# Kernel optimization log

Measured on AMD Instinct MI355X. Metric: run time of the kernel, lower is better.

## Reference

```python
import jax, jax.numpy as jnp
import numpy as np

EMBED = 128
HEADS = 32          # embed_dim // 4, forced by fuse Conv2d channel counts
HEAD_DIM = EMBED // HEADS  # 4
WS = (4, 7, 7)
N = WS[0] * WS[1] * WS[2]  # 196 tokens per window
B = 64              # batch * num_windows
SCALE = HEAD_DIM ** -0.5
EPS = 1e-5


def _rel_index():
    d, h, w = WS
    coords = np.stack(np.meshgrid(np.arange(d), np.arange(h), np.arange(w), indexing='ij'))
    flat = coords.reshape(3, -1)                       # [3, N]
    rel = (flat[:, :, None] - flat[:, None, :]).transpose(1, 2, 0).astype(np.int64)  # [N,N,3]
    rel[:, :, 0] += d - 1
    rel[:, :, 1] += h - 1
    rel[:, :, 2] += w - 1
    rel[:, :, 0] *= (2 * h - 1) * (2 * w - 1)
    rel[:, :, 1] *= (2 * w - 1)
    return rel.sum(-1).astype(np.int32)                # [N, N]


def setup_inputs() -> dict:
    key = jax.random.key(0)
    ks = jax.random.split(key, 7)
    d, h, w = WS
    tbl = (2 * d - 1) * (2 * h - 1) * (2 * w - 1)
    return {
        'x_in':      jax.random.normal(ks[0], (B, N, EMBED), dtype=jnp.float32),
        'x_in2':     jax.random.normal(ks[1], (B, N, EMBED), dtype=jnp.float32),
        'qkv_w':     jax.random.normal(ks[2], (3 * EMBED, EMBED), dtype=jnp.float32) * 0.02,
        'proj_w':    jax.random.normal(ks[3], (EMBED, EMBED), dtype=jnp.float32) * 0.02,
        'proj_b':    jnp.zeros((EMBED,), dtype=jnp.float32),
        'rpb_table': jax.random.normal(ks[4], (tbl, HEADS), dtype=jnp.float32) * 0.02,
        'fuse_w':    jax.random.normal(ks[5], (EMBED // 4, EMBED // 2), dtype=jnp.float32) * 0.1,
        'fuse_b':    jnp.zeros((EMBED // 4,), dtype=jnp.float32),
        'rel_idx':   jnp.asarray(_rel_index()),
    }


def _branch(x, qkv_w):
    b, n, c = x.shape
    qkv = (x @ qkv_w.T).reshape(b, n, 3, HEADS, c // HEADS).transpose(2, 0, 3, 1, 4)
    q, k, v = qkv[0] * SCALE, qkv[1], qkv[2]           # [b, H, n, d]
    attn = jnp.einsum('bhnd,bhmd->bhnm', q, k)         # [b, H, n, n]
    return attn, v


def reference(x_in, x_in2, qkv_w, proj_w, proj_b, rpb_table, fuse_w, fuse_b, rel_idx):
    b, n, c = x_in.shape
    attn1, v1 = _branch(x_in, qkv_w)
    attn2, v2 = _branch(x_in2, qkv_w)

    # conv-gated value fusion: Conv2d 1x1 over channel dim (= 2H) + InstanceNorm2d + ReLU + Sigmoid
    vcat = jnp.concatenate([v1, v2], axis=1)           # [b, 2H, n, d]
    v = jnp.einsum('bcnd,oc->bond', vcat, fuse_w) + fuse_b[None, :, None, None]  # [b, H, n, d]
    mu = v.mean(axis=(2, 3), keepdims=True)
    var = v.var(axis=(2, 3), keepdims=True)            # biased, as InstanceNorm2d
    v = (v - mu) * jax.lax.rsqrt(var + EPS)
    v = jax.nn.sigmoid(jax.nn.relu(v))

    # relative position bias: gather [n*n] rows of table -> [H, n, n]
    bias = rpb_table[rel_idx[:n, :n].reshape(-1)].reshape(n, n, HEADS).transpose(2, 0, 1)

    attn = jax.nn.softmax(attn1 + attn2 + bias[None], axis=-1)  # [b, H, n, n]
    x = jnp.einsum('bhnm,bhmd->bhnd', attn, v).transpose(0, 2, 1, 3).reshape(b, n, c)
    return x @ proj_w.T + proj_b
```

## Files before the change

kernel.cpp:

```cpp
#include <hip/hip_runtime.h>
#include <hip/hip_bf16.h>
#include <stdint.h>

#define NB   64
#define NTOK 196
#define NH   32
#define HD   4
#define CE   128
#define NM   38416
#define ROWS 25088

typedef __bf16 bf16x8 __attribute__((ext_vector_type(8)));
typedef float  f32x4  __attribute__((ext_vector_type(4)));

__device__ __forceinline__ float u2f(unsigned short u) {
    union { unsigned int i; float f; } z;
    z.i = ((unsigned int)u) << 16;
    return z.f;
}
__device__ __forceinline__ unsigned short f2u(float f) {
    union { float f; unsigned int i; } z; z.f = f;
    unsigned int x = z.i;
    return (unsigned short)((x + 0x7fffu + ((x >> 16) & 1u)) >> 16);
}

extern "C" __global__ __launch_bounds__(256) void qkv_gemm(
    const float* __restrict__ x1,
    const float* __restrict__ x2,
    const float* __restrict__ qkvw,
    float* __restrict__ Q, float* __restrict__ K, unsigned short* __restrict__ V)
{
    __shared__ alignas(16) unsigned short AT[64][136];
    __shared__ alignas(16) unsigned short BT[64][136];
    const int tid = threadIdx.x;
    const int r0 = blockIdx.x * 64;
    const int j0 = blockIdx.y * 64;

    for (int idx = tid; idx < 2048; idx += 256) {
        int row = idx >> 5, k0 = (idx & 31) << 2;
        int r = r0 + row;
        const float* xp = (r >= 12544) ? x2 : x1;
        int rem = r - ((r >= 12544) ? 12544 : 0);
        float4 v = *(const float4*)&xp[rem * 128 + k0];
        ushort4 u; u.x = f2u(v.x); u.y = f2u(v.y); u.z = f2u(v.z); u.w = f2u(v.w);
        *(ushort4*)&AT[row][k0] = u;
    }
    for (int idx = tid; idx < 2048; idx += 256) {
        int row = idx >> 5, k0 = (idx & 31) << 2;
        float4 v = *(const float4*)&qkvw[(j0 + row) * 128 + k0];
        ushort4 u; u.x = f2u(v.x); u.y = f2u(v.y); u.z = f2u(v.z); u.w = f2u(v.w);
        *(ushort4*)&BT[row][k0] = u;
    }
    __syncthreads();

    const int lane = tid & 63, w = tid >> 6;
    const int wm = (w >> 1) * 32, wn = (w & 1) * 32;
    const int quad = lane >> 4, tcol = lane & 15;

    f32x4 acc[2][2] = {};
#pragma unroll
    for (int ks = 0; ks < 4; ++ks) {
        int k0 = ks * 32 + quad * 8;
        bf16x8 a0 = *(const bf16x8*)&AT[wm + tcol][k0];
        bf16x8 a1 = *(const bf16x8*)&AT[wm + 16 + tcol][k0];
        bf16x8 b0 = *(const bf16x8*)&BT[wn + tcol][k0];
        bf16x8 b1 = *(const bf16x8*)&BT[wn + 16 + tcol][k0];
        acc[0][0] = __builtin_amdgcn_mfma_f32_16x16x32_bf16(a0, b0, acc[0][0], 0, 0, 0);
        acc[0][1] = __builtin_amdgcn_mfma_f32_16x16x32_bf16(a0, b1, acc[0][1], 0, 0, 0);
        acc[1][0] = __builtin_amdgcn_mfma_f32_16x16x32_bf16(a1, b0, acc[1][0], 0, 0, 0);
        acc[1][1] = __builtin_amdgcn_mfma_f32_16x16x32_bf16(a1, b1, acc[1][1], 0, 0, 0);
    }

#pragma unroll
    for (int mi = 0; mi < 2; ++mi) {
#pragma unroll
        for (int ni = 0; ni < 2; ++ni) {
            int jglob = j0 + wn + ni * 16 + tcol;
            int sel = jglob >> 7;
            int jj = jglob & 127;
            int h = jj >> 2, dd = jj & 3;
#pragma unroll
            for (int reg = 0; reg < 4; ++reg) {
                int r = r0 + wm + mi * 16 + quad * 4 + reg;
                int branch = (r >= 12544) ? 1 : 0;
                int rem = r - branch * 12544;
                int b = rem / 196;
                int n = rem - b * 196;
                float v = acc[mi][ni][reg];
                if (sel == 0) {
                    Q[((branch * 64 + b) * 32 + h) * 784 + n * 4 + dd] = v * 0.5f;
                } else if (sel == 1) {
                    K[((branch * 64 + b) * 32 + h) * 784 + n * 4 + dd] = v;
                } else {
                    V[(b * 64 + branch * 32 + h) * 784 + n * 4 + dd] = f2u(v);
                }
            }
        }
    }
}

extern "C" __global__ __launch_bounds__(256) void bias_gather(
    const int* __restrict__ rel_idx, const float* __restrict__ rpb,
    unsigned short* __restrict__ biasT)
{
    const int m = blockIdx.x;
    const int n = threadIdx.x;
    if (n >= 196) return;
    int idx = rel_idx[n * 196 + m];
    const float* row = rpb + idx * 32;
    unsigned short* o = biasT + m * 196 + n;
#pragma unroll
    for (int h = 0; h < 32; ++h)
        o[h * NM] = f2u(row[h]);
}

__device__ __forceinline__ float block_sum(float v, float* red, int tid) {
#pragma unroll
    for (int off = 32; off > 0; off >>= 1) v += __shfl_down(v, off);
    __syncthreads();
    if ((tid & 63) == 0) red[tid >> 6] = v;
    __syncthreads();
    return red[0] + red[1] + red[2] + red[3];
}

__device__ __forceinline__ float act_sig_relu(float x) {
    return x > 0.f ? __fdividef(1.f, 1.f + __expf(-x)) : 0.5f;
}

extern "C" __global__ __launch_bounds__(256) void fuse_kernel(
    const unsigned short* __restrict__ V,
    const float* __restrict__ fuse_w,
    const float* __restrict__ fuse_b,
    float* __restrict__ Vf)
{
    const int b = blockIdx.x, o0 = blockIdx.y * 2;
    const int tid = threadIdx.x;
    __shared__ float fws[2][64];
    __shared__ float red[4];
    if (tid < 128) fws[tid >> 6][tid & 63] = fuse_w[(o0 + (tid >> 6)) * 64 + (tid & 63)];
    __syncthreads();

    const unsigned short* Vb = V + b * 64 * 784;
    float a0[3] = {0.f, 0.f, 0.f}, a1[3] = {0.f, 0.f, 0.f};
    float t0 = 0.f, t1 = 0.f;
    const bool tail = tid < 16;
    for (int c = 0; c < 64; ++c) {
        float w0 = fws[0][c], w1 = fws[1][c];
        const unsigned short* Vc = Vb + c * 784;
#pragma unroll
        for (int k = 0; k < 3; ++k) {
            float x = u2f(Vc[tid + 256 * k]);
            a0[k] = fmaf(w0, x, a0[k]);
            a1[k] = fmaf(w1, x, a1[k]);
        }
        if (tail) {
            float x = u2f(Vc[tid + 768]);
            t0 = fmaf(w0, x, t0);
            t1 = fmaf(w1, x, t1);
        }
    }
    float fb0 = fuse_b[o0], fb1 = fuse_b[o0 + 1];
#pragma unroll
    for (int k = 0; k < 3; ++k) { a0[k] += fb0; a1[k] += fb1; }
    t0 += fb0; t1 += fb1;

    float s0 = a0[0] + a0[1] + a0[2] + (tail ? t0 : 0.f);
    float q0 = a0[0]*a0[0] + a0[1]*a0[1] + a0[2]*a0[2] + (tail ? t0*t0 : 0.f);
    float s1 = a1[0] + a1[1] + a1[2] + (tail ? t1 : 0.f);
    float q1 = a1[0]*a1[0] + a1[1]*a1[1] + a1[2]*a1[2] + (tail ? t1*t1 : 0.f);

    float S0 = block_sum(s0, red, tid);
    float Q0 = block_sum(q0, red, tid);
    float S1 = block_sum(s1, red, tid);
    float Q1 = block_sum(q1, red, tid);

    const float inv = 1.0f / 784.0f;
    float mu0 = S0 * inv, mu1 = S1 * inv;
    float rs0 = rsqrtf(Q0 * inv - mu0 * mu0 + 1e-5f);
    float rs1 = rsqrtf(Q1 * inv - mu1 * mu1 + 1e-5f);

    float* out0 = Vf + (b * 32 + o0) * 784;
    float* out1 = out0 + 784;
#pragma unroll
    for (int k = 0; k < 3; ++k) {
        int e = tid + 256 * k;
        out0[e] = act_sig_relu((a0[k] - mu0) * rs0);
        out1[e] = act_sig_relu((a1[k] - mu1) * rs1);
    }
    if (tail) {
        out0[tid + 768] = act_sig_relu((t0 - mu0) * rs0);
        out1[tid + 768] = act_sig_relu((t1 - mu1) * rs1);
    }
}

extern "C" __global__ __launch_bounds__(256) void attn_kernel(
    const float* __restrict__ Q, const float* __restrict__ K,
    const float* __restrict__ Vf, const unsigned short* __restrict__ biasT,
    unsigned short* __restrict__ Ob)
{
    const int bh = blockIdx.x;
    const int b = bh >> 5, h = bh & 31;
    __shared__ float k1s[196][4];
    __shared__ float k2s[196][4];
    __shared__ float vfs[196][4];
    const int tid = threadIdx.x;
    const int base1 = (b * 32 + h) * 784;
    const int base2 = ((64 + b) * 32 + h) * 784;
    const int basev = (b * 32 + h) * 784;
    for (int idx = tid; idx < 784; idx += 256) {
        (&k1s[0][0])[idx] = K[base1 + idx];
        (&k2s[0][0])[idx] = K[base2 + idx];
        (&vfs[0][0])[idx] = Vf[basev + idx];
    }
    __syncthreads();

    const int n = tid;
    if (n < 196) {
        float4 q1 = *(const float4*)(Q + base1 + n * 4);
        float4 q2 = *(const float4*)(Q + base2 + n * 4);
        const unsigned short* bp = biasT + h * NM + n;
        float S = 0.f, o0 = 0.f, o1 = 0.f, o2 = 0.f, o3 = 0.f;
        for (int m = 0; m < 196; ++m) {
            float4 k1 = *(const float4*)&k1s[m][0];
            float4 k2 = *(const float4*)&k2s[m][0];
            float s = u2f(bp[m * 196]);
            s = fmaf(q1.x, k1.x, fmaf(q1.y, k1.y, fmaf(q1.z, k1.z, fmaf(q1.w, k1.w, s))));
            s = fmaf(q2.x, k2.x, fmaf(q2.y, k2.y, fmaf(q2.z, k2.z, fmaf(q2.w, k2.w, s))));
            float p = __expf(s);
            S += p;
            float4 vv = *(const float4*)&vfs[m][0];
            o0 = fmaf(p, vv.x, o0); o1 = fmaf(p, vv.y, o1);
            o2 = fmaf(p, vv.z, o2); o3 = fmaf(p, vv.w, o3);
        }
        float invS = __fdividef(1.f, S);
        unsigned short* op = Ob + (b * 196 + n) * 128 + h * 4;
        op[0] = f2u(o0 * invS); op[1] = f2u(o1 * invS);
        op[2] = f2u(o2 * invS); op[3] = f2u(o3 * invS);
    }
}

extern "C" __global__ __launch_bounds__(256) void proj_kernel(
    const unsigned short* __restrict__ Ob, const float* __restrict__ projw,
    const float* __restrict__ projb, float* __restrict__ out)
{
    __shared__ alignas(16) unsigned short AT[64][136];
    __shared__ alignas(16) unsigned short BT[64][136];
    const int tid = threadIdx.x;
    const int r0 = blockIdx.x * 64;
    const int j0 = blockIdx.y * 64;

    for (int idx = tid; idx < 1024; idx += 256) {
        int row = idx >> 4, k0 = (idx & 15) << 3;
        *(uint4*)&AT[row][k0] = *(const uint4*)&Ob[(r0 + row) * 128 + k0];
    }
    for (int idx = tid; idx < 2048; idx += 256) {
        int row = idx >> 5, k0 = (idx & 31) << 2;
        float4 v = *(const float4*)&projw[(j0 + row) * 128 + k0];
        ushort4 u; u.x = f2u(v.x); u.y = f2u(v.y); u.z = f2u(v.z); u.w = f2u(v.w);
        *(ushort4*)&BT[row][k0] = u;
    }
    __syncthreads();

    const int lane = tid & 63, w = tid >> 6;
    const int wm = (w >> 1) * 32, wn = (w & 1) * 32;
    const int quad = lane >> 4, tcol = lane & 15;

    f32x4 acc[2][2] = {};
#pragma unroll
    for (int ks = 0; ks < 4; ++ks) {
        int k0 = ks * 32 + quad * 8;
        bf16x8 a0 = *(const bf16x8*)&AT[wm + tcol][k0];
        bf16x8 a1 = *(const bf16x8*)&AT[wm + 16 + tcol][k0];
        bf16x8 b0 = *(const bf16x8*)&BT[wn + tcol][k0];
        bf16x8 b1 = *(const bf16x8*)&BT[wn + 16 + tcol][k0];
        acc[0][0] = __builtin_amdgcn_mfma_f32_16x16x32_bf16(a0, b0, acc[0][0], 0, 0, 0);
        acc[0][1] = __builtin_amdgcn_mfma_f32_16x16x32_bf16(a0, b1, acc[0][1], 0, 0, 0);
        acc[1][0] = __builtin_amdgcn_mfma_f32_16x16x32_bf16(a1, b0, acc[1][0], 0, 0, 0);
        acc[1][1] = __builtin_amdgcn_mfma_f32_16x16x32_bf16(a1, b1, acc[1][1], 0, 0, 0);
    }

#pragma unroll
    for (int mi = 0; mi < 2; ++mi) {
#pragma unroll
        for (int ni = 0; ni < 2; ++ni) {
            int j = j0 + wn + ni * 16 + tcol;
            float pb = projb[j];
#pragma unroll
            for (int reg = 0; reg < 4; ++reg) {
                int r = r0 + wm + mi * 16 + quad * 4 + reg;
                out[r * 128 + j] = acc[mi][ni][reg] + pb;
            }
        }
    }
}

extern "C" void kernel_launch(void* const* d_in, const int* in_sizes, int n_in,
                              void* d_out, int out_size, void* d_ws, size_t ws_size,
                              hipStream_t stream)
{
    const float* x1    = (const float*)d_in[0];
    const float* x2    = (const float*)d_in[1];
    const float* qkvw  = (const float*)d_in[2];
    const float* projw = (const float*)d_in[3];
    const float* projb = (const float*)d_in[4];
    const float* rpb   = (const float*)d_in[5];
    const float* fw    = (const float*)d_in[6];
    const float* fb    = (const float*)d_in[7];
    const int*   rel   = (const int*)d_in[8];
    float* out = (float*)d_out;

    char* w = (char*)d_ws;
    float* Q            = (float*)(w);
    float* K            = (float*)(w + 12845056);
    unsigned short* V   = (unsigned short*)(w + 25690112);
    float* Vf           = (float*)(w + 32112640);
    unsigned short* bT  = (unsigned short*)(w + 38535168);
    unsigned short* Ob  = (unsigned short*)(w + 40993792);

    qkv_gemm   <<<dim3(392, 6), dim3(256), 0, stream>>>(x1, x2, qkvw, Q, K, V);
    bias_gather<<<dim3(196),    dim3(256), 0, stream>>>(rel, rpb, bT);
    fuse_kernel<<<dim3(64, 16), dim3(256), 0, stream>>>(V, fw, fb, Vf);
    attn_kernel<<<dim3(2048),   dim3(256), 0, stream>>>(Q, K, Vf, bT, Ob);
    proj_kernel<<<dim3(196, 2), dim3(256), 0, stream>>>(Ob, projw, projb, out);
}
```

Before: 177.2 us.

## Move attention to bf16 MFMA with packed Q/K and MFMA-layout bias

Rewrites the attention kernel to compute scores and P·V with 16x16x32 bf16 MFMA instructions instead of scalar FMA loops. Q and K from both branches are packed into one 8-wide bf16 row so a single MFMA does the concatenated dot product. The softmax scale and log2e are folded in so exp2 can be used. The bias is prebuilt in MFMA accumulator layout with -inf padding. A ones column in V yields the row sum for normalisation. This trades scalar ALU work and fp32 traffic for matrix-core throughput, at the cost of bf16 precision on Q, K and probabilities, plus an LDS round trip to transpose P.

```diff
diff --git a/kernel.cpp b/kernel.cpp
--- a/kernel.cpp
+++ b/kernel.cpp
@@ -8,10 +8,12 @@
 #define HD   4
 #define CE   128
 #define NM   38416
-#define ROWS 25088
 
 typedef __bf16 bf16x8 __attribute__((ext_vector_type(8)));
 typedef float  f32x4  __attribute__((ext_vector_type(4)));
+
+#define QSCALE 0.7213475204444817f
+#define LOG2E  1.4426950408889634f
 
 __device__ __forceinline__ float u2f(unsigned short u) {
     union { unsigned int i; float f; } z;
@@ -28,7 +30,8 @@
     const float* __restrict__ x1,
     const float* __restrict__ x2,
     const float* __restrict__ qkvw,
-    float* __restrict__ Q, float* __restrict__ K, unsigned short* __restrict__ V)
+    unsigned short* __restrict__ Qb, unsigned short* __restrict__ Kb,
+    unsigned short* __restrict__ V)
 {
     __shared__ alignas(16) unsigned short AT[64][136];
     __shared__ alignas(16) unsigned short BT[64][136];
@@ -88,9 +91,9 @@
                 int n = rem - b * 196;
                 float v = acc[mi][ni][reg];
                 if (sel == 0) {
-                    Q[((branch * 64 + b) * 32 + h) * 784 + n * 4 + dd] = v * 0.5f;
+                    Qb[((b * 32 + h) * 196 + n) * 8 + branch * 4 + dd] = f2u(v * QSCALE);
                 } else if (sel == 1) {
-                    K[((branch * 64 + b) * 32 + h) * 784 + n * 4 + dd] = v;
+                    Kb[((b * 32 + h) * 196 + n) * 8 + branch * 4 + dd] = f2u(v);
                 } else {
                     V[(b * 64 + branch * 32 + h) * 784 + n * 4 + dd] = f2u(v);
                 }
@@ -99,19 +102,29 @@
     }
 }
 
-extern "C" __global__ __launch_bounds__(256) void bias_gather(
+extern "C" __global__ __launch_bounds__(256) void bias_build(
     const int* __restrict__ rel_idx, const float* __restrict__ rpb,
-    unsigned short* __restrict__ biasT)
-{
-    const int m = blockIdx.x;
-    const int n = threadIdx.x;
-    if (n >= 196) return;
-    int idx = rel_idx[n * 196 + m];
-    const float* row = rpb + idx * 32;
-    unsigned short* o = biasT + m * 196 + n;
-#pragma unroll
-    for (int h = 0; h < 32; ++h)
-        o[h * NM] = f2u(row[h]);
+    unsigned short* __restrict__ biasM)
+{
+    const int qt = blockIdx.x;
+    const int h  = blockIdx.y;
+    const int tid = threadIdx.x, lane = tid & 63, wv = tid >> 6;
+    const int quad = lane >> 4, tc = lane & 15;
+    for (int nt = wv; nt < 14; nt += 4) {
+        union { uint2 v; unsigned short s[4]; } e;
+#pragma unroll
+        for (int r = 0; r < 4; ++r) {
+            int q = qt * 16 + quad * 4 + r;
+            int key = nt * 16 + tc;
+            unsigned short u = 0xFF80;
+            if (q < 196 && key < 196) {
+                int idx = rel_idx[q * 196 + key];
+                u = f2u(rpb[idx * 32 + h] * LOG2E);
+            }
+            e.s[r] = u;
+        }
+        *(uint2*)(biasM + (((h * 13 + qt) * 14 + nt) * 64 + lane) * 4) = e.v;
+    }
 }
 
 __device__ __forceinline__ float block_sum(float v, float* red, int tid) {
@@ -194,48 +207,96 @@
 }
 
 extern "C" __global__ __launch_bounds__(256) void attn_kernel(
-    const float* __restrict__ Q, const float* __restrict__ K,
-    const float* __restrict__ Vf, const unsigned short* __restrict__ biasT,
+    const unsigned short* __restrict__ Qb, const unsigned short* __restrict__ Kb,
+    const float* __restrict__ Vf, const unsigned short* __restrict__ biasM,
     unsigned short* __restrict__ Ob)
 {
     const int bh = blockIdx.x;
     const int b = bh >> 5, h = bh & 31;
-    __shared__ float k1s[196][4];
-    __shared__ float k2s[196][4];
-    __shared__ float vfs[196][4];
+    __shared__ alignas(16) unsigned short Qs[208][8];
+    __shared__ alignas(16) unsigned short Ks[224][8];
+    __shared__ alignas(16) unsigned short VT[16][232];
+    __shared__ alignas(16) float PT[4][16][36];
     const int tid = threadIdx.x;
-    const int base1 = (b * 32 + h) * 784;
-    const int base2 = ((64 + b) * 32 + h) * 784;
-    const int basev = (b * 32 + h) * 784;
-    for (int idx = tid; idx < 784; idx += 256) {
-        (&k1s[0][0])[idx] = K[base1 + idx];
-        (&k2s[0][0])[idx] = K[base2 + idx];
-        (&vfs[0][0])[idx] = Vf[basev + idx];
-    }
-    __syncthreads();
-
-    const int n = tid;
-    if (n < 196) {
-        float4 q1 = *(const float4*)(Q + base1 + n * 4);
-        float4 q2 = *(const float4*)(Q + base2 + n * 4);
-        const unsigned short* bp = biasT + h * NM + n;
-        float S = 0.f, o0 = 0.f, o1 = 0.f, o2 = 0.f, o3 = 0.f;
-        for (int m = 0; m < 196; ++m) {
-            float4 k1 = *(const float4*)&k1s[m][0];
-            float4 k2 = *(const float4*)&k2s[m][0];
-            float s = u2f(bp[m * 196]);
-            s = fmaf(q1.x, k1.x, fmaf(q1.y, k1.y, fmaf(q1.z, k1.z, fmaf(q1.w, k1.w, s))));
-            s = fmaf(q2.x, k2.x, fmaf(q2.y, k2.y, fmaf(q2.z, k2.z, fmaf(q2.w, k2.w, s))));
-            float p = __expf(s);
-            S += p;
-            float4 vv = *(const float4*)&vfs[m][0];
-            o0 = fmaf(p, vv.x, o0); o1 = fmaf(p, vv.y, o1);
-            o2 = fmaf(p, vv.z, o2); o3 = fmaf(p, vv.w, o3);
-        }
-        float invS = __fdividef(1.f, S);
-        unsigned short* op = Ob + (b * 196 + n) * 128 + h * 4;
-        op[0] = f2u(o0 * invS); op[1] = f2u(o1 * invS);
-        op[2] = f2u(o2 * invS); op[3] = f2u(o3 * invS);
+
+    const unsigned short* Qrow = Qb + bh * 196 * 8;
+    const unsigned short* Krow = Kb + bh * 196 * 8;
+    if (tid < 208) {
+        uint4 z = {0, 0, 0, 0};
+        uint4 v = (tid < 196) ? *(const uint4*)(Qrow + tid * 8) : z;
+        *(uint4*)&Qs[tid][0] = v;
+    }
+    if (tid < 224) {
+        uint4 z = {0, 0, 0, 0};
+        uint4 v = (tid < 196) ? *(const uint4*)(Krow + tid * 8) : z;
+        *(uint4*)&Ks[tid][0] = v;
+    }
+    {
+        unsigned int* vtw = (unsigned int*)&VT[0][0];
+        for (int i = tid; i < (16 * 232) / 2; i += 256) vtw[i] = 0u;
+    }
+    __syncthreads();
+    if (tid < 196) {
+        float4 vv = *(const float4*)(Vf + bh * 784 + tid * 4);
+        VT[0][tid] = f2u(vv.x); VT[1][tid] = f2u(vv.y);
+        VT[2][tid] = f2u(vv.z); VT[3][tid] = f2u(vv.w);
+        VT[4][tid] = 0x3F80;
+    }
+    __syncthreads();
+
+    const int lane = tid & 63, wv = tid >> 6;
+    const int quad = lane >> 4, tc = lane & 15;
+    float* myPT = &PT[wv][0][0];
+
+    for (int qt = wv; qt < 13; qt += 4) {
+        bf16x8 qf = *(const bf16x8*)&Qs[qt * 16 + tc][0];
+        const unsigned short* bq = biasM + (unsigned)((h * 13 + qt) * 14) * 256;
+        f32x4 Oacc = {};
+#pragma unroll 1
+        for (int kt = 0; kt < 7; ++kt) {
+#pragma unroll
+            for (int half = 0; half < 2; ++half) {
+                int nt = kt * 2 + half;
+                bf16x8 kf = {};
+                if (quad == 0) kf = *(const bf16x8*)&Ks[nt * 16 + tc][0];
+                uint2 bw = *(const uint2*)(bq + nt * 256 + lane * 4);
+                f32x4 s;
+                union { unsigned int u; float f; } c0, c1, c2, c3;
+                c0.u = bw.x << 16; c1.u = bw.x & 0xffff0000u;
+                c2.u = bw.y << 16; c3.u = bw.y & 0xffff0000u;
+                s[0] = c0.f; s[1] = c1.f; s[2] = c2.f; s[3] = c3.f;
+                s = __builtin_amdgcn_mfma_f32_16x16x32_bf16(qf, kf, s, 0, 0, 0);
+                float p0 = exp2f(s[0]), p1 = exp2f(s[1]);
+                float p2 = exp2f(s[2]), p3 = exp2f(s[3]);
+                int col = half * 16 + tc;
+                myPT[(quad * 4 + 0) * 36 + col] = p0;
+                myPT[(quad * 4 + 1) * 36 + col] = p1;
+                myPT[(quad * 4 + 2) * 36 + col] = p2;
+                myPT[(quad * 4 + 3) * 36 + col] = p3;
+            }
+            float4 pa = *(const float4*)&myPT[tc * 36 + quad * 8];
+            float4 pb = *(const float4*)&myPT[tc * 36 + quad * 8 + 4];
+            bf16x8 pf;
+            pf[0] = (__bf16)pa.x; pf[1] = (__bf16)pa.y;
+            pf[2] = (__bf16)pa.z; pf[3] = (__bf16)pa.w;
+            pf[4] = (__bf16)pb.x; pf[5] = (__bf16)pb.y;
+            pf[6] = (__bf16)pb.z; pf[7] = (__bf16)pb.w;
+            bf16x8 vfr = *(const bf16x8*)&VT[tc][kt * 32 + quad * 8];
+            Oacc = __builtin_amdgcn_mfma_f32_16x16x32_bf16(pf, vfr, Oacc, 0, 0, 0);
+        }
+        int srcLane = quad * 16 + 4;
+        float r0 = __shfl(Oacc[0], srcLane);
+        float r1 = __shfl(Oacc[1], srcLane);
+        float r2 = __shfl(Oacc[2], srcLane);
+        float r3 = __shfl(Oacc[3], srcLane);
+        if (tc < 4) {
+            int qbase = qt * 16 + quad * 4;
+            unsigned short* op = Ob + (b * 196 + qbase) * 128 + h * 4 + tc;
+            if (qbase + 0 < 196) op[0 * 128] = f2u(Oacc[0] * __builtin_amdgcn_rcpf(r0));
+            if (qbase + 1 < 196) op[1 * 128] = f2u(Oacc[1] * __builtin_amdgcn_rcpf(r1));
+            if (qbase + 2 < 196) op[2 * 128] = f2u(Oacc[2] * __builtin_amdgcn_rcpf(r2));
+            if (qbase + 3 < 196) op[3 * 128] = f2u(Oacc[3] * __builtin_amdgcn_rcpf(r3));
+        }
     }
 }
 
@@ -310,16 +371,16 @@
     float* out = (float*)d_out;
 
     char* w = (char*)d_ws;
-    float* Q            = (float*)(w);
-    float* K            = (float*)(w + 12845056);
-    unsigned short* V   = (unsigned short*)(w + 25690112);
-    float* Vf           = (float*)(w + 32112640);
-    unsigned short* bT  = (unsigned short*)(w + 38535168);
-    unsigned short* Ob  = (unsigned short*)(w + 40993792);
-
-    qkv_gemm   <<<dim3(392, 6), dim3(256), 0, stream>>>(x1, x2, qkvw, Q, K, V);
-    bias_gather<<<dim3(196),    dim3(256), 0, stream>>>(rel, rpb, bT);
+    unsigned short* Qb  = (unsigned short*)(w);
+    unsigned short* Kb  = (unsigned short*)(w + 6422528);
+    unsigned short* V   = (unsigned short*)(w + 12845056);
+    float*          Vf  = (float*)(w + 19267584);
+    unsigned short* bM  = (unsigned short*)(w + 25690112);
+    unsigned short* Ob  = (unsigned short*)(w + 28672000);
+
+    qkv_gemm  <<<dim3(392, 6), dim3(256), 0, stream>>>(x1, x2, qkvw, Qb, Kb, V);
+    bias_build<<<dim3(13, 32), dim3(256), 0, stream>>>(rel, rpb, bM);
     fuse_kernel<<<dim3(64, 16), dim3(256), 0, stream>>>(V, fw, fb, Vf);
-    attn_kernel<<<dim3(2048),   dim3(256), 0, stream>>>(Q, K, Vf, bT, Ob);
+    attn_kernel<<<dim3(2048),   dim3(256), 0, stream>>>(Qb, Kb, Vf, bM, Ob);
     proj_kernel<<<dim3(196, 2), dim3(256), 0, stream>>>(Ob, projw, projb, out);
 }
```

New measurement: 189.2 us. 6.8% more time.
